# Kernel tuning notes

Measured on AMD Instinct MI355X. Metric: run time of the kernel, lower is better.

Reference implementation:

```python
import jax, jax.numpy as jnp
import numpy as np
from jax import lax

RES = [8, 12, 20, 18, 32]
C = 4            # n_features
NCELLS = 2
DOMAIN = (0.0, 1.0, 0.0, 1.0)
NPTS = 1000000


def depthwise_conv3x3(a, w):
    # a: (Ncells, C, R, R); w: (C, 1, 3, 3) depthwise (groups=C), padding=1, no bias
    return lax.conv_general_dilated(
        a, w, window_strides=(1, 1), padding='SAME',
        dimension_numbers=('NCHW', 'OIHW', 'NCHW'), feature_group_count=C)


def grid_sample_2d(feat, gx, gy):
    # Custom bilinear grid sample with per-cell half-cell offsets (offset=True).
    # feat: (Ncells, C, IH, IW); gx, gy: (N,) normalized coords in [-1, 1].
    n_cells, c, ih, iw = feat.shape
    ix = (gx + 1.0) * 0.5 * (iw - 1)          # pixel coords, align_corners=True
    iy = (gy + 1.0) * 0.5 * (ih - 1)
    off = jnp.arange(n_cells, dtype=feat.dtype) / n_cells  # staggered cells
    ix = ix[None, :] + off[:, None]            # (Ncells, N)
    iy = iy[None, :] + off[:, None]
    ix0 = jnp.floor(ix)
    iy0 = jnp.floor(iy)
    wx = ix - ix0                              # fractional weights (unclamped)
    wy = iy - iy0
    x0 = jnp.clip(ix0.astype(jnp.int32), 0, iw - 1)
    x1 = jnp.clip(ix0.astype(jnp.int32) + 1, 0, iw - 1)
    y0 = jnp.clip(iy0.astype(jnp.int32), 0, ih - 1)
    y1 = jnp.clip(iy0.astype(jnp.int32) + 1, 0, ih - 1)
    flat = feat.reshape(n_cells, c, ih * iw)

    def gather(yy, xx):
        idx = yy * iw + xx                      # (Ncells, N)
        return jnp.take_along_axis(flat, idx[:, None, :], axis=2)  # (Ncells, C, N)

    nw = gather(y0, x0)
    ne = gather(y0, x1)
    sw = gather(y1, x0)
    se = gather(y1, x1)
    w_nw = ((1 - wx) * (1 - wy))[:, None, :]
    w_ne = (wx * (1 - wy))[:, None, :]
    w_sw = ((1 - wx) * wy)[:, None, :]
    w_se = (wx * wy)[:, None, :]
    return nw * w_nw + ne * w_ne + sw * w_sw + se * w_se  # (Ncells, C, N)


def encode_level(alpha, conv_w, gx, gy):
    a = jnp.tanh(depthwise_conv3x3(alpha, conv_w))
    s = grid_sample_2d(a, gx, gy)               # (Ncells, C, N)
    return s.sum(0).T                           # (N, C) == F.sum(0).view(C,-1).t()


def setup_inputs() -> dict:
    key = jax.random.key(0)
    kx, ky, kw = jax.random.split(key, 3)
    inp = {
        'x': jax.random.uniform(kx, (NPTS, 1), dtype=jnp.float32),
        'y': jax.random.uniform(ky, (NPTS, 1), dtype=jnp.float32),
        'conv_w': jax.random.normal(kw, (C, 1, 3, 3), dtype=jnp.float32) * 0.3,
    }
    for i, r in enumerate(RES):
        inp[f'F{i}'] = jax.random.uniform(
            jax.random.fold_in(key, i + 10), (NCELLS, C, r, r),
            dtype=jnp.float32, minval=-1e-5, maxval=1e-5)
    return inp


def reference(x, y, F0, F1, F2, F3, F4, conv_w):
    x_min, x_max, y_min, y_max = DOMAIN
    gx = ((x - x_min) / (x_max - x_min)) * 2.0 - 1.0   # (N,1)
    gy = ((y - y_min) / (y_max - y_min)) * 2.0 - 1.0
    gx = gx[:, 0]
    gy = gy[:, 0]
    feats = [encode_level(F, conv_w, gx, gy) for F in (F0, F1, F2, F3, F4)]
    return jnp.concatenate(feats, axis=1)              # (N, 5*C)
```

## Files before the change

### kernel.cpp

```cpp
#include <hip/hip_runtime.h>
#include <cmath>


#define NTH 512
#define PPT 4

constexpr int TOT = 15648;
#define OFF0 0
#define OFF1 512
#define OFF2 1664
#define OFF3 4864
#define OFF4 7456

template<int R>
__device__ __forceinline__ void conv_level(const float* __restrict__ F,
                                           const float* __restrict__ w,
                                           float* __restrict__ dst,
                                           int tid, int nth)
{
    const int n = 8 * R * R;
    for (int i = tid; i < n; i += nth) {
        int c    = i & 3;
        int pos  = i >> 2;
        int cell = (pos >= R * R) ? 1 : 0;
        int rem  = pos - cell * R * R;
        int yy   = rem / R;
        int xx   = rem - yy * R;
        const float* Fc = F + (cell * 4 + c) * R * R;
        float acc = 0.f;
#pragma unroll
        for (int ky = 0; ky < 3; ++ky) {
#pragma unroll
            for (int kx = 0; kx < 3; ++kx) {
                int sy = yy + ky - 1, sx = xx + kx - 1;
                if ((unsigned)sy < (unsigned)R && (unsigned)sx < (unsigned)R)
                    acc += w[c * 9 + ky * 3 + kx] * Fc[sy * R + sx];
            }
        }
        dst[cell * (R * R * 4) + (yy * R + xx) * 4 + c] = tanhf(acc);
    }
}

__global__ void conv_kernel(const float* __restrict__ F0, const float* __restrict__ F1,
                            const float* __restrict__ F2, const float* __restrict__ F3,
                            const float* __restrict__ F4, const float* __restrict__ w,
                            float* __restrict__ tab)
{
    int tid = blockIdx.x * blockDim.x + threadIdx.x;
    int nth = gridDim.x * blockDim.x;
    conv_level<8 >(F0, w, tab + OFF0, tid, nth);
    conv_level<12>(F1, w, tab + OFF1, tid, nth);
    conv_level<20>(F2, w, tab + OFF2, tid, nth);
    conv_level<18>(F3, w, tab + OFF3, tid, nth);
    conv_level<32>(F4, w, tab + OFF4, tid, nth);
}

template<int R>
__device__ __forceinline__ float4 sample_level(const float* __restrict__ lt,
                                               float px, float py)
{
    float fx = px * (float)(R - 1);
    float fy = py * (float)(R - 1);
    float4 acc = make_float4(0.f, 0.f, 0.f, 0.f);
#pragma unroll
    for (int cell = 0; cell < 2; ++cell) {
        float ixc = fx + 0.5f * (float)cell;
        float iyc = fy + 0.5f * (float)cell;
        float fx0 = floorf(ixc);
        float fy0 = floorf(iyc);
        float wx = ixc - fx0;
        float wy = iyc - fy0;
        int ix0 = (int)fx0;
        int iy0 = (int)fy0;
        int x0 = min(max(ix0,     0), R - 1);
        int x1 = min(max(ix0 + 1, 0), R - 1);
        int y0 = min(max(iy0,     0), R - 1);
        int y1 = min(max(iy0 + 1, 0), R - 1);
        const float* cb = lt + cell * (R * R * 4);
        float4 nw = *(const float4*)(cb + (y0 * R + x0) * 4);
        float4 ne = *(const float4*)(cb + (y0 * R + x1) * 4);
        float4 sw = *(const float4*)(cb + (y1 * R + x0) * 4);
        float4 se = *(const float4*)(cb + (y1 * R + x1) * 4);
        float u = 1.f - wx, v = 1.f - wy;
        float wnw = u * v, wne = wx * v, wsw = u * wy, wse = wx * wy;
        acc.x = fmaf(wnw, nw.x, acc.x); acc.x = fmaf(wne, ne.x, acc.x);
        acc.x = fmaf(wsw, sw.x, acc.x); acc.x = fmaf(wse, se.x, acc.x);
        acc.y = fmaf(wnw, nw.y, acc.y); acc.y = fmaf(wne, ne.y, acc.y);
        acc.y = fmaf(wsw, sw.y, acc.y); acc.y = fmaf(wse, se.y, acc.y);
        acc.z = fmaf(wnw, nw.z, acc.z); acc.z = fmaf(wne, ne.z, acc.z);
        acc.z = fmaf(wsw, sw.z, acc.z); acc.z = fmaf(wse, se.z, acc.z);
        acc.w = fmaf(wnw, nw.w, acc.w); acc.w = fmaf(wne, ne.w, acc.w);
        acc.w = fmaf(wsw, sw.w, acc.w); acc.w = fmaf(wse, se.w, acc.w);
    }
    return acc;
}

__device__ __forceinline__ void sample_body(const float* lds,
                                            const float* __restrict__ x,
                                            const float* __restrict__ y,
                                            float* __restrict__ out, int npts)
{
    int p0 = blockIdx.x * (NTH * PPT) + threadIdx.x;
    float pxs[PPT], pys[PPT];
#pragma unroll
    for (int k = 0; k < PPT; ++k) {
        int p = p0 + k * NTH;
        int pc = (p < npts) ? p : 0;
        pxs[k] = x[pc];
        pys[k] = y[pc];
    }
    for (int k = 0; k < PPT; ++k) {
        int p = p0 + k * NTH;
        float px = pxs[k];
        float py = pys[k];
        float4 r0 = sample_level<8 >(lds + OFF0, px, py);
        float4 r1 = sample_level<12>(lds + OFF1, px, py);
        float4 r2 = sample_level<20>(lds + OFF2, px, py);
        float4 r3 = sample_level<18>(lds + OFF3, px, py);
        float4 r4 = sample_level<32>(lds + OFF4, px, py);
        if (p < npts) {
            float4* op = (float4*)(out + (size_t)p * 20);
            op[0] = r0; op[1] = r1; op[2] = r2; op[3] = r3; op[4] = r4;
        }
    }
}

__global__ __launch_bounds__(NTH, 4) void sample_kernel(const float* __restrict__ x,
                                                        const float* __restrict__ y,
                                                        const float* __restrict__ tab,
                                                        float* __restrict__ out, int npts)
{
    __shared__ __align__(16) float lds[TOT];
    const float4* g4 = (const float4*)tab;
    float4* l4 = (float4*)lds;
    for (int i = threadIdx.x; i < TOT / 4; i += NTH)
        l4[i] = g4[i];
    __syncthreads();
    sample_body(lds, x, y, out, npts);
}

__global__ __launch_bounds__(NTH, 4) void fused_kernel(const float* __restrict__ x,
                                                       const float* __restrict__ y,
                                                       const float* __restrict__ F0,
                                                       const float* __restrict__ F1,
                                                       const float* __restrict__ F2,
                                                       const float* __restrict__ F3,
                                                       const float* __restrict__ F4,
                                                       const float* __restrict__ w,
                                                       float* __restrict__ out, int npts)
{
    __shared__ __align__(16) float lds[TOT];
    conv_level<8 >(F0, w, lds + OFF0, threadIdx.x, NTH);
    conv_level<12>(F1, w, lds + OFF1, threadIdx.x, NTH);
    conv_level<20>(F2, w, lds + OFF2, threadIdx.x, NTH);
    conv_level<18>(F3, w, lds + OFF3, threadIdx.x, NTH);
    conv_level<32>(F4, w, lds + OFF4, threadIdx.x, NTH);
    __syncthreads();
    sample_body(lds, x, y, out, npts);
}

extern "C" void kernel_launch(void* const* d_in, const int* in_sizes, int n_in,
                              void* d_out, int out_size, void* d_ws, size_t ws_size,
                              hipStream_t stream)
{
    const float* x  = (const float*)d_in[0];
    const float* y  = (const float*)d_in[1];
    const float* w  = (const float*)d_in[2];
    const float* F0 = (const float*)d_in[3];
    const float* F1 = (const float*)d_in[4];
    const float* F2 = (const float*)d_in[5];
    const float* F3 = (const float*)d_in[6];
    const float* F4 = (const float*)d_in[7];
    float* out = (float*)d_out;
    int npts = in_sizes[0];

    int nb = (npts + NTH * PPT - 1) / (NTH * PPT);

    if (ws_size >= (size_t)TOT * sizeof(float)) {
        float* tab = (float*)d_ws;
        conv_kernel<<<(TOT + 255) / 256, 256, 0, stream>>>(F0, F1, F2, F3, F4, w, tab);
        sample_kernel<<<nb, NTH, 0, stream>>>(x, y, tab, out, npts);
    } else {
        fused_kernel<<<nb, NTH, 0, stream>>>(x, y, F0, F1, F2, F3, F4, w, out, npts);
    }
}
```

Baseline: 124.8 us.

## Store conv table in fp16 in LDS and raise occupancy

Converts the tanh(conv) lookup table to half precision, halving LDS footprint (about 31 KB per block instead of about 62 KB) and halving the bytes read per corner gather, which are unpacked to float on load. Points per thread drop from 4 to 2 and the occupancy hint goes from 4 to 8 blocks, so more waves can hide LDS latency, at the cost of more blocks each reloading the table. Results are written directly, and out-of-range points are skipped. The risk is precision loss in the table values, which are outputs of tanh in [-1,1] and here have tiny magnitudes.

```diff
diff --git a/kernel.cpp b/kernel.cpp
--- a/kernel.cpp
+++ b/kernel.cpp
@@ -1,9 +1,10 @@
 #include <hip/hip_runtime.h>
+#include <hip/hip_fp16.h>
 #include <cmath>
 
 
 #define NTH 512
-#define PPT 4
+#define PPT 2
 
 constexpr int TOT = 15648;
 #define OFF0 0
@@ -15,7 +16,7 @@
 template<int R>
 __device__ __forceinline__ void conv_level(const float* __restrict__ F,
                                            const float* __restrict__ w,
-                                           float* __restrict__ dst,
+                                           __half* __restrict__ dst,
                                            int tid, int nth)
 {
     const int n = 8 * R * R;
@@ -37,14 +38,14 @@
                     acc += w[c * 9 + ky * 3 + kx] * Fc[sy * R + sx];
             }
         }
-        dst[cell * (R * R * 4) + (yy * R + xx) * 4 + c] = tanhf(acc);
+        dst[cell * (R * R * 4) + (yy * R + xx) * 4 + c] = __float2half(tanhf(acc));
     }
 }
 
 __global__ void conv_kernel(const float* __restrict__ F0, const float* __restrict__ F1,
                             const float* __restrict__ F2, const float* __restrict__ F3,
                             const float* __restrict__ F4, const float* __restrict__ w,
-                            float* __restrict__ tab)
+                            __half* __restrict__ tab)
 {
     int tid = blockIdx.x * blockDim.x + threadIdx.x;
     int nth = gridDim.x * blockDim.x;
@@ -55,8 +56,18 @@
     conv_level<32>(F4, w, tab + OFF4, tid, nth);
 }
 
+__device__ __forceinline__ float4 corner_fetch(const __half* __restrict__ p)
+{
+    uint2 raw = *(const uint2*)p;
+    __half2 lo = *(__half2*)&raw.x;
+    __half2 hi = *(__half2*)&raw.y;
+    float2 f01 = __half22float2(lo);
+    float2 f23 = __half22float2(hi);
+    return make_float4(f01.x, f01.y, f23.x, f23.y);
+}
+
 template<int R>
-__device__ __forceinline__ float4 sample_level(const float* __restrict__ lt,
+__device__ __forceinline__ float4 sample_level(const __half* __restrict__ lt,
                                                float px, float py)
 {
     float fx = px * (float)(R - 1);
@@ -76,11 +87,11 @@
         int x1 = min(max(ix0 + 1, 0), R - 1);
         int y0 = min(max(iy0,     0), R - 1);
         int y1 = min(max(iy0 + 1, 0), R - 1);
-        const float* cb = lt + cell * (R * R * 4);
-        float4 nw = *(const float4*)(cb + (y0 * R + x0) * 4);
-        float4 ne = *(const float4*)(cb + (y0 * R + x1) * 4);
-        float4 sw = *(const float4*)(cb + (y1 * R + x0) * 4);
-        float4 se = *(const float4*)(cb + (y1 * R + x1) * 4);
+        const __half* cb = lt + cell * (R * R * 4);
+        float4 nw = corner_fetch(cb + (y0 * R + x0) * 4);
+        float4 ne = corner_fetch(cb + (y0 * R + x1) * 4);
+        float4 sw = corner_fetch(cb + (y1 * R + x0) * 4);
+        float4 se = corner_fetch(cb + (y1 * R + x1) * 4);
         float u = 1.f - wx, v = 1.f - wy;
         float wnw = u * v, wne = wx * v, wsw = u * wy, wse = wx * wy;
         acc.x = fmaf(wnw, nw.x, acc.x); acc.x = fmaf(wne, ne.x, acc.x);
@@ -95,7 +106,7 @@
     return acc;
 }
 
-__device__ __forceinline__ void sample_body(const float* lds,
+__device__ __forceinline__ void sample_body(const __half* lds,
                                             const float* __restrict__ x,
                                             const float* __restrict__ y,
                                             float* __restrict__ out, int npts)
@@ -109,31 +120,30 @@
         pxs[k] = x[pc];
         pys[k] = y[pc];
     }
+#pragma unroll
     for (int k = 0; k < PPT; ++k) {
         int p = p0 + k * NTH;
+        if (p >= npts) continue;
         float px = pxs[k];
         float py = pys[k];
-        float4 r0 = sample_level<8 >(lds + OFF0, px, py);
-        float4 r1 = sample_level<12>(lds + OFF1, px, py);
-        float4 r2 = sample_level<20>(lds + OFF2, px, py);
-        float4 r3 = sample_level<18>(lds + OFF3, px, py);
-        float4 r4 = sample_level<32>(lds + OFF4, px, py);
-        if (p < npts) {
-            float4* op = (float4*)(out + (size_t)p * 20);
-            op[0] = r0; op[1] = r1; op[2] = r2; op[3] = r3; op[4] = r4;
-        }
+        float4* op = (float4*)(out + (size_t)p * 20);
+        op[0] = sample_level<8 >(lds + OFF0, px, py);
+        op[1] = sample_level<12>(lds + OFF1, px, py);
+        op[2] = sample_level<20>(lds + OFF2, px, py);
+        op[3] = sample_level<18>(lds + OFF3, px, py);
+        op[4] = sample_level<32>(lds + OFF4, px, py);
     }
 }
 
-__global__ __launch_bounds__(NTH, 4) void sample_kernel(const float* __restrict__ x,
+__global__ __launch_bounds__(NTH, 8) void sample_kernel(const float* __restrict__ x,
                                                         const float* __restrict__ y,
-                                                        const float* __restrict__ tab,
+                                                        const __half* __restrict__ tab,
                                                         float* __restrict__ out, int npts)
 {
-    __shared__ __align__(16) float lds[TOT];
-    const float4* g4 = (const float4*)tab;
-    float4* l4 = (float4*)lds;
-    for (int i = threadIdx.x; i < TOT / 4; i += NTH)
+    __shared__ __align__(16) __half lds[TOT];
+    const uint4* g4 = (const uint4*)tab;
+    uint4* l4 = (uint4*)lds;
+    for (int i = threadIdx.x; i < TOT * 2 / 16; i += NTH)
         l4[i] = g4[i];
     __syncthreads();
     sample_body(lds, x, y, out, npts);
@@ -149,7 +159,7 @@
                                                        const float* __restrict__ w,
                                                        float* __restrict__ out, int npts)
 {
-    __shared__ __align__(16) float lds[TOT];
+    __shared__ __align__(16) __half lds[TOT];
     conv_level<8 >(F0, w, lds + OFF0, threadIdx.x, NTH);
     conv_level<12>(F1, w, lds + OFF1, threadIdx.x, NTH);
     conv_level<20>(F2, w, lds + OFF2, threadIdx.x, NTH);
@@ -176,8 +186,8 @@
 
     int nb = (npts + NTH * PPT - 1) / (NTH * PPT);
 
-    if (ws_size >= (size_t)TOT * sizeof(float)) {
-        float* tab = (float*)d_ws;
+    if (ws_size >= (size_t)TOT * sizeof(__half)) {
+        __half* tab = (__half*)d_ws;
         conv_kernel<<<(TOT + 255) / 256, 256, 0, stream>>>(F0, F1, F2, F3, F4, w, tab);
         sample_kernel<<<nb, NTH, 0, stream>>>(x, y, tab, out, npts);
     } else {
```

New measurement: 125.0 us. About the same (+0.2%).
